# Optimization experiments

Hardware: AMD Instinct MI355X
Metric: run time of the kernel (lower is better)

Reference implementation:

```python
import jax, jax.numpy as jnp
import numpy as np

B = 8
A = 180      # num_angles
D = 512      # det_count
IMG = 512    # img_size


def _forward(x):
    # --- Ram-Lak filter in frequency domain ---
    freq = jnp.abs(jnp.fft.rfftfreq(D)).astype(jnp.float32)            # [D//2+1]
    filtered = jnp.fft.irfft(jnp.fft.rfft(x, axis=-1) * freq, n=D, axis=-1)  # [B,A,D]

    # --- precompute per-angle detector coordinates for every pixel ---
    lin = jnp.linspace(-1.0, 1.0, IMG, dtype=jnp.float32)
    yy, xx = jnp.meshgrid(lin, lin, indexing='ij')
    xxf = xx.reshape(-1)                                               # [HW]
    yyf = yy.reshape(-1)
    angles = jnp.linspace(0.0, np.pi - np.pi / A, A, dtype=jnp.float32)
    t = (xxf[None, :] * jnp.cos(angles)[:, None]
         + yyf[None, :] * jnp.sin(angles)[:, None]) / np.sqrt(2.0)     # [A,HW]
    u = jnp.clip((t + 1.0) * 0.5 * (D - 1.0), 0.0, D - 1.0)
    idx0 = jnp.floor(u).astype(jnp.int32)
    idx1 = jnp.minimum(idx0 + 1, D - 1)
    w = u - idx0.astype(jnp.float32)

    # --- backprojection sweep: scan over angles, accumulate in-register ---
    proj = jnp.transpose(filtered, (1, 0, 2))                          # [A,B,D]

    def step(acc, inputs):
        p, i0, i1, wa = inputs                                         # p:[B,D], i*/wa:[HW]
        s = jnp.take(p, i0, axis=1) * (1.0 - wa) + jnp.take(p, i1, axis=1) * wa
        return acc + s, None

    bn = x.shape[0]
    acc0 = jnp.zeros((bn, IMG * IMG), dtype=jnp.float32)
    acc, _ = jax.lax.scan(step, acc0, (proj, idx0, idx1, w))

    det_pixel_size = 2.0 / float(D)
    fbp = acc.reshape(bn, 1, IMG, IMG) * (det_pixel_size * np.pi / float(A))

    # --- 3x3 gaussian blur (sigma=0.5), depthwise on single channel ---
    coords = jnp.arange(-1, 2, dtype=jnp.float32)
    k1 = jnp.exp(-0.5 * (coords / 0.5) ** 2)
    k1 = k1 / k1.sum()
    k2 = jnp.outer(k1, k1)[None, None]                                 # [1,1,3,3] OIHW
    fbp = jax.lax.conv_general_dilated(fbp, k2, (1, 1), 'SAME')
    return jnp.clip(fbp, -1.0, 1.0)


def setup_inputs() -> dict:
    key = jax.random.key(0)
    x = jax.random.normal(key, (B, A, D), dtype=jnp.float32)
    return {"x": x, "input_is_sinogram": 1}


def reference(x, input_is_sinogram):
    # input_is_sinogram is a constant flag (True path): x is the sinogram [B,A,D].
    return _forward(x)
```

## Files before the change

### kernel.cpp

```cpp
#include <hip/hip_runtime.h>
#include <hip/hip_fp16.h>
#include <math.h>

#define NDET 512
#define NANG 180
#define NB   8
#define NIMG 512

#define WS_CASA 0
#define WS_CBT  360
#define WS_FGH  46464
#define WS_BP   (46464 + 368640)

typedef _Float16 h2_t __attribute__((ext_vector_type(2)));

__device__ __forceinline__ int hswz(int s) {
    return (s & 0x78) | ((s ^ (s >> 3)) & 7);
}

__global__ __launch_bounds__(256) void k_filter(const float* __restrict__ x, float* ws) {
    __shared__ float xs[8 * 516];
    __shared__ float hrs[512];
    const int a     = blockIdx.x >> 1;
    const int half_ = blockIdx.x & 1;
    const int tid   = threadIdx.x;
    const int lane  = tid & 63;
    const int wv    = tid >> 6;

    #pragma unroll
    for (int p = 0; p < 2; ++p) {
        int n = tid + 256 * p;
        float h;
        if (n == 0) h = 0.25f;
        else if ((n & 1) == 0) h = 0.0f;
        else {
            int m = min(n, 512 - n);
            float s = __sinf((float)m * (float)(M_PI / 512.0));
            h = -1.0f / (262144.0f * s * s);
        }
        hrs[hswz(n >> 2) * 4 + (n & 3)] = h;
    }
    {
        int b  = wv * 2 + (lane >> 5);
        int l5 = lane & 31;
        const float* xr = x + (b * NANG + a) * NDET;
        float* xd = xs + b * 516;
        #pragma unroll
        for (int p = 0; p < 4; ++p) {
            int idx = l5 * 4 + p * 128;
            *(float4*)(xd + idx) = *(const float4*)(xr + idx);
        }
    }
    if (half_ == 0) {
        double th = (double)a * (M_PI / 180.0);
        double sc = 255.5 / sqrt(2.0);
        const float ca = (float)(cos(th) * sc), sa = (float)(sin(th) * sc);
        if (tid == 0) {
            ws[WS_CASA + 2 * a]     = ca;
            ws[WS_CASA + 2 * a + 1] = sa;
        }
        const int bx = tid & 15, by = tid >> 4;
        const float x0 = -1.f + (float)(bx * 32)      * (2.f / 511.f);
        const float x1 = -1.f + (float)(bx * 32 + 31) * (2.f / 511.f);
        const float y0 = -1.f + (float)(by * 32)      * (2.f / 511.f);
        const float y1 = -1.f + (float)(by * 32 + 31) * (2.f / 511.f);
        float u00 = fmaf(x0, ca, fmaf(y0, sa, 255.5f));
        float u01 = fmaf(x1, ca, fmaf(y0, sa, 255.5f));
        float u10 = fmaf(x0, ca, fmaf(y1, sa, 255.5f));
        float u11 = fmaf(x1, ca, fmaf(y1, sa, 255.5f));
        float umin = fminf(fminf(u00, u01), fminf(u10, u11));
        int d0 = (int)floorf(umin);
        d0 = max(0, min(NDET - 34, d0));
        ws[WS_CBT + tid * 180 + a] = 255.5f - (float)d0;
    }
    __syncthreads();

    const int b  = lane & 7;
    const int t  = lane >> 3;
    const int n0 = half_ * 256 + wv * 64 + t * 8;
    const int q  = n0 >> 2;
    const float* xrow = xs + b * 516;

    float acc[8] = {0, 0, 0, 0, 0, 0, 0, 0};
    float win[12];
    {
        int s2 = (-q - 2) & 127;
        int s1 = (-q - 1) & 127;
        float4 h2 = *(const float4*)(hrs + hswz(s2) * 4);
        float4 h1 = *(const float4*)(hrs + hswz(s1) * 4);
        win[0] = h2.x; win[1] = h2.y; win[2]  = h2.z; win[3]  = h2.w;
        win[4] = h1.x; win[5] = h1.y; win[6]  = h1.z; win[7]  = h1.w;
    }
    #pragma unroll 2
    for (int c = 0; c < 128; ++c) {
        int s = (c - q) & 127;
        float4 hc = *(const float4*)(hrs + hswz(s) * 4);
        win[8] = hc.x; win[9] = hc.y; win[10] = hc.z; win[11] = hc.w;
        float4 xv = *(const float4*)(xrow + c * 4);
        float xa[4] = {xv.x, xv.y, xv.z, xv.w};
        #pragma unroll
        for (int k = 0; k < 8; ++k)
            #pragma unroll
            for (int j = 0; j < 4; ++j)
                acc[k] = fmaf(xa[j], win[8 + j - k], acc[k]);
        #pragma unroll
        for (int i2 = 0; i2 < 8; ++i2) win[i2] = win[i2 + 4];
    }
    __half* fgh = (__half*)(ws + WS_FGH);
    #pragma unroll
    for (int k = 0; k < 8; ++k)
        fgh[(a * NDET + n0 + k) * NB + b] = __float2half(acc[k]);
}

#define WWE  33
#define CHA  60
#define ECH  (CHA * WWE)

#define PERM_LO 0x05040100u
#define PERM_HI 0x07060302u

__global__ __launch_bounds__(1024, 4) void k_bp(float* ws) {
    __shared__ uint4 win4[2][2 * ECH];
    const int tid  = threadIdx.x;
    const int wv   = tid >> 6, lane = tid & 63;
    const int tile = blockIdx.x;
    const int bx   = tile & 15, by = tile >> 4;
    const int iy   = by * 32 + (wv >> 2) * 8 + (lane >> 3);
    const int ix   = bx * 32 + (wv & 3) * 8 + (lane & 7);
    const float xf = -1.0f + (float)ix * (2.0f / 511.0f);
    const float yf = -1.0f + (float)iy * (2.0f / 511.0f);

    const __half* __restrict__ fgh  = (const __half*)(ws + WS_FGH);
    const float*  __restrict__ cbt  = ws + WS_CBT + tile * 180;
    const float*  __restrict__ casa = ws + WS_CASA;

    const int e0 = tid, e1 = tid + 1024;
    uint4 sA0, sB0, sA1, sB1;

    auto sload = [&](int ch) {
        {
            int a = e0 / 33, j = e0 - a * 33, ag = ch * CHA + a;
            int d0 = (int)(255.5f - cbt[ag]);
            const uint4* s = (const uint4*)(fgh + (ag * NDET + d0 + j) * NB);
            sA0 = s[0]; sB0 = s[1];
        }
        if (e1 < ECH) {
            int a = e1 / 33, j = e1 - a * 33, ag = ch * CHA + a;
            int d0 = (int)(255.5f - cbt[ag]);
            const uint4* s = (const uint4*)(fgh + (ag * NDET + d0 + j) * NB);
            sA1 = s[0]; sB1 = s[1];
        }
    };
    auto swrite = [&](int buf) {
        uint4 ra, rb;
        ra.x = __builtin_amdgcn_perm(sB0.x, sA0.x, PERM_LO);
        ra.y = __builtin_amdgcn_perm(sB0.x, sA0.x, PERM_HI);
        ra.z = __builtin_amdgcn_perm(sB0.y, sA0.y, PERM_LO);
        ra.w = __builtin_amdgcn_perm(sB0.y, sA0.y, PERM_HI);
        rb.x = __builtin_amdgcn_perm(sB0.z, sA0.z, PERM_LO);
        rb.y = __builtin_amdgcn_perm(sB0.z, sA0.z, PERM_HI);
        rb.z = __builtin_amdgcn_perm(sB0.w, sA0.w, PERM_LO);
        rb.w = __builtin_amdgcn_perm(sB0.w, sA0.w, PERM_HI);
        win4[buf][e0] = ra; win4[buf][ECH + e0] = rb;
        if (e1 < ECH) {
            uint4 rc, rd;
            rc.x = __builtin_amdgcn_perm(sB1.x, sA1.x, PERM_LO);
            rc.y = __builtin_amdgcn_perm(sB1.x, sA1.x, PERM_HI);
            rc.z = __builtin_amdgcn_perm(sB1.y, sA1.y, PERM_LO);
            rc.w = __builtin_amdgcn_perm(sB1.y, sA1.y, PERM_HI);
            rd.x = __builtin_amdgcn_perm(sB1.z, sA1.z, PERM_LO);
            rd.y = __builtin_amdgcn_perm(sB1.z, sA1.z, PERM_HI);
            rd.z = __builtin_amdgcn_perm(sB1.w, sA1.w, PERM_LO);
            rd.w = __builtin_amdgcn_perm(sB1.w, sA1.w, PERM_HI);
            win4[buf][e1] = rc; win4[buf][ECH + e1] = rd;
        }
    };

    float acc[8] = {0, 0, 0, 0, 0, 0, 0, 0};
    auto comp = [&](int buf, int ch) {
        const uint4* base = &win4[buf][0];
        #pragma unroll 4
        for (int al = 0; al < CHA; ++al) {
            const int ag = ch * CHA + al;
            const float2 cs = *(const float2*)(casa + 2 * ag);
            const float  cb = cbt[ag];
            float v = fmaf(xf, cs.x, fmaf(yf, cs.y, cb));
            v = __builtin_amdgcn_fmed3f(v, 0.0f, 32.99996948f);
            float fj = floorf(v);
            float w  = v - fj;
            int  j0  = (int)fj;
            const uint4* p = base + al * WWE + j0;
            uint4 dA = p[0];
            uint4 dB = p[ECH];
            h2_t wp = __builtin_bit_cast(h2_t, __builtin_amdgcn_cvt_pkrtz(1.0f - w, w));
            acc[0] = __builtin_amdgcn_fdot2(__builtin_bit_cast(h2_t, dA.x), wp, acc[0], false);
            acc[1] = __builtin_amdgcn_fdot2(__builtin_bit_cast(h2_t, dA.y), wp, acc[1], false);
            acc[2] = __builtin_amdgcn_fdot2(__builtin_bit_cast(h2_t, dA.z), wp, acc[2], false);
            acc[3] = __builtin_amdgcn_fdot2(__builtin_bit_cast(h2_t, dA.w), wp, acc[3], false);
            acc[4] = __builtin_amdgcn_fdot2(__builtin_bit_cast(h2_t, dB.x), wp, acc[4], false);
            acc[5] = __builtin_amdgcn_fdot2(__builtin_bit_cast(h2_t, dB.y), wp, acc[5], false);
            acc[6] = __builtin_amdgcn_fdot2(__builtin_bit_cast(h2_t, dB.z), wp, acc[6], false);
            acc[7] = __builtin_amdgcn_fdot2(__builtin_bit_cast(h2_t, dB.w), wp, acc[7], false);
        }
    };

    sload(0); swrite(0); __syncthreads();
    sload(1); comp(0, 0); swrite(1); __syncthreads();
    sload(2); comp(1, 1); swrite(0); __syncthreads();
    comp(0, 2);

    const float scale = (float)((2.0 / 512.0) * M_PI / 180.0);
    float* bp = ws + WS_BP;
    #pragma unroll
    for (int b = 0; b < 8; ++b)
        bp[b * (NIMG * NIMG) + iy * NIMG + ix] = acc[b] * scale;
}

__global__ __launch_bounds__(256) void k_blur(const float* __restrict__ ws, float* __restrict__ out) {
    const int gid = blockIdx.x * 256 + threadIdx.x;
    const int b  = gid >> 18;
    const int r  = (gid >> 9) & 511;
    const int cx = gid & 511;
    const float KA = 0.10650697891920077f;
    const float KB = 0.78698604216159850f;
    const float* img = ws + WS_BP + b * (NIMG * NIMG);
    const float* rp = img + r * 512 + cx;

    float rowm = 0.0f, row0, rowp = 0.0f;
    {
        float l  = (cx > 0)   ? rp[-1] : 0.0f;
        float rr = (cx < 511) ? rp[1]  : 0.0f;
        row0 = KA * (l + rr) + KB * rp[0];
    }
    if (r > 0) {
        const float* q = rp - 512;
        float l  = (cx > 0)   ? q[-1] : 0.0f;
        float rr = (cx < 511) ? q[1]  : 0.0f;
        rowm = KA * (l + rr) + KB * q[0];
    }
    if (r < 511) {
        const float* q = rp + 512;
        float l  = (cx > 0)   ? q[-1] : 0.0f;
        float rr = (cx < 511) ? q[1]  : 0.0f;
        rowp = KA * (l + rr) + KB * q[0];
    }
    float v = KA * (rowm + rowp) + KB * row0;
    v = fminf(fmaxf(v, -1.0f), 1.0f);
    out[gid] = v;
}

extern "C" void kernel_launch(void* const* d_in, const int* in_sizes, int n_in,
                              void* d_out, int out_size, void* d_ws, size_t ws_size,
                              hipStream_t stream) {
    const float* x = (const float*)d_in[0];
    float* out = (float*)d_out;
    float* ws  = (float*)d_ws;

    k_filter<<<NANG * 2, 256, 0, stream>>>(x, ws);
    k_bp<<<256, 1024, 0, stream>>>(ws);
    k_blur<<<(NB * NIMG * NIMG) / 256, 256, 0, stream>>>(ws, out);
}
```

Before: 68.61 us.

## Fuse filter and backprojection into one persistent kernel with grid barrier

```diff
diff --git a/kernel.cpp b/kernel.cpp
--- a/kernel.cpp
+++ b/kernel.cpp
@@ -6,214 +6,226 @@
 #define NANG 180
 #define NB   8
 #define NIMG 512
-
-#define WS_CASA 0
-#define WS_CBT  360
-#define WS_FGH  46464
-#define WS_BP   (46464 + 368640)
+#define NBLK 256
+
+#define WS_CNT  0
+#define WS_FGA  4
+#define WS_FGB  (4 + 368640)
+#define WS_BP   (4 + 737280)
 
 typedef _Float16 h2_t __attribute__((ext_vector_type(2)));
+
+__device__ __forceinline__ void gld_lds16(const void* g, void* l) {
+    __builtin_amdgcn_global_load_lds((__attribute__((address_space(1))) void*)g,
+                                     (__attribute__((address_space(3))) void*)l,
+                                     16, 0, 0);
+}
 
 __device__ __forceinline__ int hswz(int s) {
     return (s & 0x78) | ((s ^ (s >> 3)) & 7);
 }
 
-__global__ __launch_bounds__(256) void k_filter(const float* __restrict__ x, float* ws) {
-    __shared__ float xs[8 * 516];
-    __shared__ float hrs[512];
-    const int a     = blockIdx.x >> 1;
-    const int half_ = blockIdx.x & 1;
-    const int tid   = threadIdx.x;
-    const int lane  = tid & 63;
-    const int wv    = tid >> 6;
-
-    #pragma unroll
-    for (int p = 0; p < 2; ++p) {
-        int n = tid + 256 * p;
-        float h;
-        if (n == 0) h = 0.25f;
-        else if ((n & 1) == 0) h = 0.0f;
-        else {
-            int m = min(n, 512 - n);
-            float s = __sinf((float)m * (float)(M_PI / 512.0));
-            h = -1.0f / (262144.0f * s * s);
-        }
-        hrs[hswz(n >> 2) * 4 + (n & 3)] = h;
-    }
-    {
-        int b  = wv * 2 + (lane >> 5);
-        int l5 = lane & 31;
-        const float* xr = x + (b * NANG + a) * NDET;
-        float* xd = xs + b * 516;
-        #pragma unroll
-        for (int p = 0; p < 4; ++p) {
-            int idx = l5 * 4 + p * 128;
-            *(float4*)(xd + idx) = *(const float4*)(xr + idx);
-        }
-    }
-    if (half_ == 0) {
-        double th = (double)a * (M_PI / 180.0);
+__device__ __forceinline__ void gbar(int* c, int tid) {
+    __threadfence();
+    __syncthreads();
+    if (tid == 0) {
+        __hip_atomic_fetch_add(c, 1, __ATOMIC_ACQ_REL, __HIP_MEMORY_SCOPE_AGENT);
+        while (__hip_atomic_load(c, __ATOMIC_ACQUIRE, __HIP_MEMORY_SCOPE_AGENT) < NBLK)
+            __builtin_amdgcn_s_sleep(2);
+    }
+    __syncthreads();
+    __threadfence();
+}
+
+#define WWE  33
+#define CHA  60
+#define ECH  (CHA * WWE)
+
+__global__ __launch_bounds__(1024, 4) void k_fused(const float* __restrict__ x, float* ws) {
+    __shared__ uint4 win4[2][2 * ECH];
+    __shared__ float casal[2 * NANG];
+    __shared__ float cbl[NANG];
+    float* smem = (float*)win4;
+    const int bid = blockIdx.x;
+    const int tid = threadIdx.x;
+    int* cnt = (int*)(ws + WS_CNT);
+
+    if (tid < NANG) {
+        double th = (double)tid * (M_PI / 180.0);
         double sc = 255.5 / sqrt(2.0);
-        const float ca = (float)(cos(th) * sc), sa = (float)(sin(th) * sc);
-        if (tid == 0) {
-            ws[WS_CASA + 2 * a]     = ca;
-            ws[WS_CASA + 2 * a + 1] = sa;
-        }
-        const int bx = tid & 15, by = tid >> 4;
+        const float cad = (float)(cos(th) * sc), sad = (float)(sin(th) * sc);
+        casal[2 * tid]     = cad;
+        casal[2 * tid + 1] = sad;
+        const int bx = bid & 15, by = bid >> 4;
         const float x0 = -1.f + (float)(bx * 32)      * (2.f / 511.f);
         const float x1 = -1.f + (float)(bx * 32 + 31) * (2.f / 511.f);
         const float y0 = -1.f + (float)(by * 32)      * (2.f / 511.f);
         const float y1 = -1.f + (float)(by * 32 + 31) * (2.f / 511.f);
-        float u00 = fmaf(x0, ca, fmaf(y0, sa, 255.5f));
-        float u01 = fmaf(x1, ca, fmaf(y0, sa, 255.5f));
-        float u10 = fmaf(x0, ca, fmaf(y1, sa, 255.5f));
-        float u11 = fmaf(x1, ca, fmaf(y1, sa, 255.5f));
+        float u00 = fmaf(x0, cad, fmaf(y0, sad, 255.5f));
+        float u01 = fmaf(x1, cad, fmaf(y0, sad, 255.5f));
+        float u10 = fmaf(x0, cad, fmaf(y1, sad, 255.5f));
+        float u11 = fmaf(x1, cad, fmaf(y1, sad, 255.5f));
         float umin = fminf(fminf(u00, u01), fminf(u10, u11));
         int d0 = (int)floorf(umin);
         d0 = max(0, min(NDET - 34, d0));
-        ws[WS_CBT + tid * 180 + a] = 255.5f - (float)d0;
-    }
-    __syncthreads();
-
-    const int b  = lane & 7;
-    const int t  = lane >> 3;
-    const int n0 = half_ * 256 + wv * 64 + t * 8;
-    const int q  = n0 >> 2;
-    const float* xrow = xs + b * 516;
-
-    float acc[8] = {0, 0, 0, 0, 0, 0, 0, 0};
-    float win[12];
+        cbl[tid] = 255.5f - (float)d0;
+    }
+
+    if (bid < NANG) {
+        float* xs  = smem;
+        float* hrs = smem + 8 * 516;
+        float* fsm = smem + 8 * 516 + 512;
+        const int a = bid;
+        if (tid < 512) {
+            const int lane = tid & 63;
+            const int wv   = tid >> 6;
+            {
+                int n = tid;
+                float h;
+                if (n == 0) h = 0.25f;
+                else if ((n & 1) == 0) h = 0.0f;
+                else {
+                    int m = min(n, 512 - n);
+                    float s = __sinf((float)m * (float)(M_PI / 512.0));
+                    h = -1.0f / (262144.0f * s * s);
+                }
+                hrs[hswz(n >> 2) * 4 + (n & 3)] = h;
+            }
+            {
+                const float* xr = x + (wv * NANG + a) * NDET;
+                float* xd = xs + wv * 516;
+                *(float4*)(xd + lane * 4)       = *(const float4*)(xr + lane * 4);
+                *(float4*)(xd + 256 + lane * 4) = *(const float4*)(xr + 256 + lane * 4);
+            }
+        }
+        __syncthreads();
+        if (tid < 512) {
+            const int lane = tid & 63;
+            const int wv   = tid >> 6;
+            const int b  = lane & 7;
+            const int t  = lane >> 3;
+            const int n0 = wv * 64 + t * 8;
+            const int q  = n0 >> 2;
+            const float* xrow = xs + b * 516;
+
+            float acc[8] = {0, 0, 0, 0, 0, 0, 0, 0};
+            float win[12];
+            {
+                int s2 = (-q - 2) & 127;
+                int s1 = (-q - 1) & 127;
+                float4 h2 = *(const float4*)(hrs + hswz(s2) * 4);
+                float4 h1 = *(const float4*)(hrs + hswz(s1) * 4);
+                win[0] = h2.x; win[1] = h2.y; win[2]  = h2.z; win[3]  = h2.w;
+                win[4] = h1.x; win[5] = h1.y; win[6]  = h1.z; win[7]  = h1.w;
+            }
+            #pragma unroll 2
+            for (int c = 0; c < 128; ++c) {
+                int s = (c - q) & 127;
+                float4 hc = *(const float4*)(hrs + hswz(s) * 4);
+                win[8] = hc.x; win[9] = hc.y; win[10] = hc.z; win[11] = hc.w;
+                float4 xv = *(const float4*)(xrow + c * 4);
+                float xa[4] = {xv.x, xv.y, xv.z, xv.w};
+                #pragma unroll
+                for (int k = 0; k < 8; ++k)
+                    #pragma unroll
+                    for (int j = 0; j < 4; ++j)
+                        acc[k] = fmaf(xa[j], win[8 + j - k], acc[k]);
+                #pragma unroll
+                for (int i2 = 0; i2 < 8; ++i2) win[i2] = win[i2 + 4];
+            }
+            #pragma unroll
+            for (int k = 0; k < 8; ++k)
+                fsm[(n0 + k) * 8 + b] = acc[k];
+        }
+        __syncthreads();
+        if (tid < 512) {
+            const int d  = tid;
+            const int d1 = min(d + 1, NDET - 1);
+            const float* A  = fsm + d * 8;
+            const float* Bv = fsm + d1 * 8;
+            uint4 eA, eB;
+            unsigned wds[8];
+            #pragma unroll
+            for (int b = 0; b < 8; ++b) {
+                __half2 h;
+                h.x = __float2half(A[b]);
+                h.y = __float2half(Bv[b]);
+                wds[b] = __builtin_bit_cast(unsigned, h);
+            }
+            eA.x = wds[0]; eA.y = wds[1]; eA.z = wds[2]; eA.w = wds[3];
+            eB.x = wds[4]; eB.y = wds[5]; eB.z = wds[6]; eB.w = wds[7];
+            *(uint4*)((char*)(ws + WS_FGA) + (a * NDET + d) * 16) = eA;
+            *(uint4*)((char*)(ws + WS_FGB) + (a * NDET + d) * 16) = eB;
+        }
+    }
+    gbar(cnt, tid);
+
     {
-        int s2 = (-q - 2) & 127;
-        int s1 = (-q - 1) & 127;
-        float4 h2 = *(const float4*)(hrs + hswz(s2) * 4);
-        float4 h1 = *(const float4*)(hrs + hswz(s1) * 4);
-        win[0] = h2.x; win[1] = h2.y; win[2]  = h2.z; win[3]  = h2.w;
-        win[4] = h1.x; win[5] = h1.y; win[6]  = h1.z; win[7]  = h1.w;
-    }
-    #pragma unroll 2
-    for (int c = 0; c < 128; ++c) {
-        int s = (c - q) & 127;
-        float4 hc = *(const float4*)(hrs + hswz(s) * 4);
-        win[8] = hc.x; win[9] = hc.y; win[10] = hc.z; win[11] = hc.w;
-        float4 xv = *(const float4*)(xrow + c * 4);
-        float xa[4] = {xv.x, xv.y, xv.z, xv.w};
+        const int tile = bid;
+        const int wv   = tid >> 6, lane = tid & 63;
+        const int bx   = tile & 15, by = tile >> 4;
+        const int iy   = by * 32 + (wv >> 2) * 8 + (lane >> 3);
+        const int ix   = bx * 32 + (wv & 3) * 8 + (lane & 7);
+        const float xf = -1.0f + (float)ix * (2.0f / 511.0f);
+        const float yf = -1.0f + (float)iy * (2.0f / 511.0f);
+
+        const char* __restrict__ fga = (const char*)(ws + WS_FGA);
+        const char* __restrict__ fgb = (const char*)(ws + WS_FGB);
+
+        auto stageq = [&](int buf, int ch) {
+            #pragma unroll
+            for (int r = 0; r < 4; ++r) {
+                int c = r * 1024 + tid;
+                if (c < 2 * ECH) {
+                    int reg = c / ECH;
+                    int e   = c - reg * ECH;
+                    int a   = e / 33;
+                    int o   = e - a * 33;
+                    int ag  = ch * CHA + a;
+                    int d0  = (int)(255.5f - cbl[ag]);
+                    const char* g = (reg ? fgb : fga) + (ag * NDET + d0 + o) * 16;
+                    gld_lds16(g, (char*)(&win4[buf][0]) + c * 16);
+                }
+            }
+        };
+
+        float acc[8] = {0, 0, 0, 0, 0, 0, 0, 0};
+        auto comp = [&](int buf, int ch) {
+            #pragma unroll 4
+            for (int al = 0; al < CHA; ++al) {
+                const int ag = ch * CHA + al;
+                const float ca = casal[2 * ag], sa = casal[2 * ag + 1];
+                const float cb = cbl[ag];
+                float v = fmaf(xf, ca, fmaf(yf, sa, cb));
+                v = __builtin_amdgcn_fmed3f(v, 0.0f, 32.99996948f);
+                float fj = floorf(v);
+                float w  = v - fj;
+                int  j0  = (int)fj;
+                uint4 dA = win4[buf][al * WWE + j0];
+                uint4 dB = win4[buf][ECH + al * WWE + j0];
+                h2_t wp = __builtin_bit_cast(h2_t, __builtin_amdgcn_cvt_pkrtz(1.0f - w, w));
+                acc[0] = __builtin_amdgcn_fdot2(__builtin_bit_cast(h2_t, dA.x), wp, acc[0], false);
+                acc[1] = __builtin_amdgcn_fdot2(__builtin_bit_cast(h2_t, dA.y), wp, acc[1], false);
+                acc[2] = __builtin_amdgcn_fdot2(__builtin_bit_cast(h2_t, dA.z), wp, acc[2], false);
+                acc[3] = __builtin_amdgcn_fdot2(__builtin_bit_cast(h2_t, dA.w), wp, acc[3], false);
+                acc[4] = __builtin_amdgcn_fdot2(__builtin_bit_cast(h2_t, dB.x), wp, acc[4], false);
+                acc[5] = __builtin_amdgcn_fdot2(__builtin_bit_cast(h2_t, dB.y), wp, acc[5], false);
+                acc[6] = __builtin_amdgcn_fdot2(__builtin_bit_cast(h2_t, dB.z), wp, acc[6], false);
+                acc[7] = __builtin_amdgcn_fdot2(__builtin_bit_cast(h2_t, dB.w), wp, acc[7], false);
+            }
+        };
+
+        stageq(0, 0); __syncthreads();
+        stageq(1, 1); comp(0, 0); __syncthreads();
+        stageq(0, 2); comp(1, 1); __syncthreads();
+        comp(0, 2);
+
+        const float scale = (float)((2.0 / 512.0) * M_PI / 180.0);
+        float* bp = ws + WS_BP;
         #pragma unroll
-        for (int k = 0; k < 8; ++k)
-            #pragma unroll
-            for (int j = 0; j < 4; ++j)
-                acc[k] = fmaf(xa[j], win[8 + j - k], acc[k]);
-        #pragma unroll
-        for (int i2 = 0; i2 < 8; ++i2) win[i2] = win[i2 + 4];
-    }
-    __half* fgh = (__half*)(ws + WS_FGH);
-    #pragma unroll
-    for (int k = 0; k < 8; ++k)
-        fgh[(a * NDET + n0 + k) * NB + b] = __float2half(acc[k]);
-}
-
-#define WWE  33
-#define CHA  60
-#define ECH  (CHA * WWE)
-
-#define PERM_LO 0x05040100u
-#define PERM_HI 0x07060302u
-
-__global__ __launch_bounds__(1024, 4) void k_bp(float* ws) {
-    __shared__ uint4 win4[2][2 * ECH];
-    const int tid  = threadIdx.x;
-    const int wv   = tid >> 6, lane = tid & 63;
-    const int tile = blockIdx.x;
-    const int bx   = tile & 15, by = tile >> 4;
-    const int iy   = by * 32 + (wv >> 2) * 8 + (lane >> 3);
-    const int ix   = bx * 32 + (wv & 3) * 8 + (lane & 7);
-    const float xf = -1.0f + (float)ix * (2.0f / 511.0f);
-    const float yf = -1.0f + (float)iy * (2.0f / 511.0f);
-
-    const __half* __restrict__ fgh  = (const __half*)(ws + WS_FGH);
-    const float*  __restrict__ cbt  = ws + WS_CBT + tile * 180;
-    const float*  __restrict__ casa = ws + WS_CASA;
-
-    const int e0 = tid, e1 = tid + 1024;
-    uint4 sA0, sB0, sA1, sB1;
-
-    auto sload = [&](int ch) {
-        {
-            int a = e0 / 33, j = e0 - a * 33, ag = ch * CHA + a;
-            int d0 = (int)(255.5f - cbt[ag]);
-            const uint4* s = (const uint4*)(fgh + (ag * NDET + d0 + j) * NB);
-            sA0 = s[0]; sB0 = s[1];
-        }
-        if (e1 < ECH) {
-            int a = e1 / 33, j = e1 - a * 33, ag = ch * CHA + a;
-            int d0 = (int)(255.5f - cbt[ag]);
-            const uint4* s = (const uint4*)(fgh + (ag * NDET + d0 + j) * NB);
-            sA1 = s[0]; sB1 = s[1];
-        }
-    };
-    auto swrite = [&](int buf) {
-        uint4 ra, rb;
-        ra.x = __builtin_amdgcn_perm(sB0.x, sA0.x, PERM_LO);
-        ra.y = __builtin_amdgcn_perm(sB0.x, sA0.x, PERM_HI);
-        ra.z = __builtin_amdgcn_perm(sB0.y, sA0.y, PERM_LO);
-        ra.w = __builtin_amdgcn_perm(sB0.y, sA0.y, PERM_HI);
-        rb.x = __builtin_amdgcn_perm(sB0.z, sA0.z, PERM_LO);
-        rb.y = __builtin_amdgcn_perm(sB0.z, sA0.z, PERM_HI);
-        rb.z = __builtin_amdgcn_perm(sB0.w, sA0.w, PERM_LO);
-        rb.w = __builtin_amdgcn_perm(sB0.w, sA0.w, PERM_HI);
-        win4[buf][e0] = ra; win4[buf][ECH + e0] = rb;
-        if (e1 < ECH) {
-            uint4 rc, rd;
-            rc.x = __builtin_amdgcn_perm(sB1.x, sA1.x, PERM_LO);
-            rc.y = __builtin_amdgcn_perm(sB1.x, sA1.x, PERM_HI);
-            rc.z = __builtin_amdgcn_perm(sB1.y, sA1.y, PERM_LO);
-            rc.w = __builtin_amdgcn_perm(sB1.y, sA1.y, PERM_HI);
-            rd.x = __builtin_amdgcn_perm(sB1.z, sA1.z, PERM_LO);
-            rd.y = __builtin_amdgcn_perm(sB1.z, sA1.z, PERM_HI);
-            rd.z = __builtin_amdgcn_perm(sB1.w, sA1.w, PERM_LO);
-            rd.w = __builtin_amdgcn_perm(sB1.w, sA1.w, PERM_HI);
-            win4[buf][e1] = rc; win4[buf][ECH + e1] = rd;
-        }
-    };
-
-    float acc[8] = {0, 0, 0, 0, 0, 0, 0, 0};
-    auto comp = [&](int buf, int ch) {
-        const uint4* base = &win4[buf][0];
-        #pragma unroll 4
-        for (int al = 0; al < CHA; ++al) {
-            const int ag = ch * CHA + al;
-            const float2 cs = *(const float2*)(casa + 2 * ag);
-            const float  cb = cbt[ag];
-            float v = fmaf(xf, cs.x, fmaf(yf, cs.y, cb));
-            v = __builtin_amdgcn_fmed3f(v, 0.0f, 32.99996948f);
-            float fj = floorf(v);
-            float w  = v - fj;
-            int  j0  = (int)fj;
-            const uint4* p = base + al * WWE + j0;
-            uint4 dA = p[0];
-            uint4 dB = p[ECH];
-            h2_t wp = __builtin_bit_cast(h2_t, __builtin_amdgcn_cvt_pkrtz(1.0f - w, w));
-            acc[0] = __builtin_amdgcn_fdot2(__builtin_bit_cast(h2_t, dA.x), wp, acc[0], false);
-            acc[1] = __builtin_amdgcn_fdot2(__builtin_bit_cast(h2_t, dA.y), wp, acc[1], false);
-            acc[2] = __builtin_amdgcn_fdot2(__builtin_bit_cast(h2_t, dA.z), wp, acc[2], false);
-            acc[3] = __builtin_amdgcn_fdot2(__builtin_bit_cast(h2_t, dA.w), wp, acc[3], false);
-            acc[4] = __builtin_amdgcn_fdot2(__builtin_bit_cast(h2_t, dB.x), wp, acc[4], false);
-            acc[5] = __builtin_amdgcn_fdot2(__builtin_bit_cast(h2_t, dB.y), wp, acc[5], false);
-            acc[6] = __builtin_amdgcn_fdot2(__builtin_bit_cast(h2_t, dB.z), wp, acc[6], false);
-            acc[7] = __builtin_amdgcn_fdot2(__builtin_bit_cast(h2_t, dB.w), wp, acc[7], false);
-        }
-    };
-
-    sload(0); swrite(0); __syncthreads();
-    sload(1); comp(0, 0); swrite(1); __syncthreads();
-    sload(2); comp(1, 1); swrite(0); __syncthreads();
-    comp(0, 2);
-
-    const float scale = (float)((2.0 / 512.0) * M_PI / 180.0);
-    float* bp = ws + WS_BP;
-    #pragma unroll
-    for (int b = 0; b < 8; ++b)
-        bp[b * (NIMG * NIMG) + iy * NIMG + ix] = acc[b] * scale;
+        for (int b = 0; b < 8; ++b)
+            bp[b * (NIMG * NIMG) + iy * NIMG + ix] = acc[b] * scale;
+    }
 }
 
 __global__ __launch_bounds__(256) void k_blur(const float* __restrict__ ws, float* __restrict__ out) {
@@ -256,7 +268,7 @@
     float* out = (float*)d_out;
     float* ws  = (float*)d_ws;
 
-    k_filter<<<NANG * 2, 256, 0, stream>>>(x, ws);
-    k_bp<<<256, 1024, 0, stream>>>(ws);
+    hipMemsetAsync(ws + WS_CNT, 0, 16, stream);
+    k_fused<<<NBLK, 1024, 0, stream>>>(x, ws);
     k_blur<<<(NB * NIMG * NIMG) / 256, 256, 0, stream>>>(ws, out);
 }
```

New measurement: 223.7 us. +226.0%, slower.
